# Kernel tuning notes

Hardware: AMD Instinct MI355X
Metric: run time of the kernel (lower is better)

The kernel has to match this reference:

```python
import jax, jax.numpy as jnp
import numpy as np

N = 100000
E = 1600000
IN_DIM = 128
HID = 128
C = 10
N_INJ = 20000
T_HET = 0.5          # self.hetero_level (set by set_adaptation_from_data)
HP_MAX = 1.0         # highpass_scale_max
INJ_LAM = 0.8        # self.inject_lambda


def setup_inputs() -> dict:
    key = jax.random.key(0)
    ks = jax.random.split(key, 16)
    glorot = lambda k, i, o: jax.random.normal(k, (i, o), jnp.float32) * (2.0 / (i + o)) ** 0.5
    return {
        "x": jax.random.normal(ks[0], (N, IN_DIM), jnp.float32),
        "edge_index": jax.random.randint(ks[1], (2, E), 0, N, jnp.int64),
        "inject_indices": jax.random.randint(ks[2], (N_INJ,), 0, N, jnp.int64),
        "initial_preds": jax.random.uniform(ks[3], (N, C), jnp.float32),
        "W1": glorot(ks[4], IN_DIM, HID), "b1": jnp.zeros((HID,), jnp.float32),
        "W2": glorot(ks[5], HID, HID),   "b2": jnp.zeros((HID,), jnp.float32),
        "Wl1": glorot(ks[6], IN_DIM, HID),
        "Wl2": glorot(ks[7], HID, HID),
        "Wm1": glorot(ks[8], HID, HID), "bm1": jnp.zeros((HID,), jnp.float32),
        "Wm2": glorot(ks[9], HID, C),   "bm2": jnp.zeros((C,), jnp.float32),
    }


def _gcn_norm(edge_index):
    # add self loops, symmetric D^{-1/2} (A+I) D^{-1/2} normalization (PyG GCNConv default)
    loops = jnp.arange(N, dtype=edge_index.dtype)
    src = jnp.concatenate([edge_index[0], loops])
    dst = jnp.concatenate([edge_index[1], loops])
    deg = jax.ops.segment_sum(jnp.ones_like(dst, jnp.float32), dst, num_segments=N)
    dinv = jnp.where(deg > 0, jax.lax.rsqrt(jnp.maximum(deg, 1.0)), 0.0)
    norm = dinv[src] * dinv[dst]  # [E+N]
    return src, dst, norm


def _gcn_conv(x, W, b, src, dst, norm):
    h = x @ W                                   # [N, H]
    msg = h[src] * norm[:, None]                # gather + scale, [E+N, H]
    return jax.ops.segment_sum(msg, dst, num_segments=N) + b


def reference(x, edge_index, inject_indices, initial_preds,
              W1, b1, W2, b2, Wl1, Wl2, Wm1, bm1, Wm2, bm2):
    src, dst, norm = _gcn_norm(edge_index)
    mix = T_HET * HP_MAX

    low1 = _gcn_conv(x, W1, b1, src, dst, norm)
    high1 = x @ Wl1 - low1
    h = jax.nn.relu(low1 + mix * high1)        # dropout: eval mode (identity)

    low2 = _gcn_conv(h, W2, b2, src, dst, norm)
    high2 = h @ Wl2 - low2
    h2 = low2 + mix * high2

    logits = jax.nn.relu(h2 @ Wm1 + bm1) @ Wm2 + bm2   # [N, C]
    # indexed injection: logits[idx] = logits[idx] + lam * preds[idx]
    logits = logits.at[inject_indices].set(
        logits[inject_indices] + INJ_LAM * initial_preds[inject_indices])
    return jax.nn.log_softmax(logits, axis=1)
```

## Files before the change

### kernel.cpp

```cpp
#include <hip/hip_runtime.h>
#include <hip/hip_bf16.h>
#include <math.h>

typedef __attribute__((ext_vector_type(8))) short short8;
typedef __attribute__((ext_vector_type(4))) float f32x4;
typedef __attribute__((ext_vector_type(2))) float f32x2;

#define INJ_LAM 0.8f
#define BSH 9
#define BWD 512

__device__ inline float bf2f(unsigned short s){
  union{unsigned u; float f;} v; v.u=((unsigned)s)<<16; return v.f;
}
__device__ inline unsigned short f2bf(float f){
  __hip_bfloat16 h=__float2bfloat16(f);
  return *reinterpret_cast<unsigned short*>(&h);
}
__device__ inline unsigned pack2(float lo, float hi){
  return ((unsigned)f2bf(hi)<<16)|(unsigned)f2bf(lo);
}

__global__ void k_bhist(const int* __restrict__ dst, unsigned* __restrict__ bhist8,
                        const int* __restrict__ inj, unsigned char* __restrict__ flag,
                        int E, int NI){
  __shared__ unsigned lh[256];
  int t=threadIdx.x;
  lh[t]=0u;
  int i=blockIdx.x*256+t;
  if(i<NI) flag[inj[i]]=1;
  __syncthreads();
  int base=blockIdx.x*2048;
  #pragma unroll
  for(int k=0;k<8;k++){
    int e=base+k*256+t;
    if(e<E) atomicAdd(&lh[dst[e]>>BSH],1u);
  }
  __syncthreads();
  if(lh[t]) atomicAdd(&bhist8[t*8],lh[t]);
}

__global__ void k_bscan(const unsigned* __restrict__ bhist8, unsigned* __restrict__ bbase,
                        unsigned* __restrict__ bcur8, int NBK){
  __shared__ unsigned ss[256];
  int t=threadIdx.x;
  unsigned v=(t<NBK)?bhist8[t*8]:0u;
  ss[t]=v; __syncthreads();
  for(int off=1;off<256;off<<=1){
    unsigned u=(t>=off)?ss[t-off]:0u; __syncthreads();
    ss[t]+=u; __syncthreads();
  }
  unsigned excl=ss[t]-v;
  if(t<NBK){ bbase[t]=excl; bcur8[t*8]=excl; }
  if(t==255) bbase[NBK]=ss[255];
}

__global__ void k_bscatter(const int* __restrict__ src, const int* __restrict__ dst,
                           unsigned* __restrict__ bcur8,
                           int* __restrict__ psrc, int* __restrict__ pdst, int E){
  __shared__ unsigned lh[256];
  __shared__ unsigned gb[256];
  int t=threadIdx.x;
  lh[t]=0u; __syncthreads();
  int base=blockIdx.x*2048;
  unsigned lr[8]; int bk[8], sv[8], dv_[8];
  #pragma unroll
  for(int k=0;k<8;k++){
    int e=base+k*256+t;
    if(e<E){
      int d=dst[e]; int b=d>>BSH;
      bk[k]=b; dv_[k]=d; sv[k]=src[e];
      lr[k]=atomicAdd(&lh[b],1u);
    } else bk[k]=-1;
  }
  __syncthreads();
  if(lh[t]) gb[t]=atomicAdd(&bcur8[t*8],lh[t]);
  __syncthreads();
  #pragma unroll
  for(int k=0;k<8;k++){
    if(bk[k]>=0){
      unsigned p=gb[bk[k]]+lr[k];
      psrc[p]=sv[k]; pdst[p]=dv_[k];
    }
  }
}

__launch_bounds__(256)
__global__ void k_bucket(const int* __restrict__ psrc, const int* __restrict__ pdst,
                         const unsigned* __restrict__ bbase, unsigned* __restrict__ rank,
                         unsigned* __restrict__ meta,
                         float* __restrict__ dinv, int* __restrict__ csr, int N){
  __shared__ unsigned lc[BWD];
  __shared__ unsigned lo[BWD];
  __shared__ unsigned ss[256];
  int b=blockIdx.x, t=threadIdx.x;
  unsigned e0=bbase[b], e1=bbase[b+1];
  int lo_node=b<<BSH;
  lc[t]=0u; lc[t+256]=0u; __syncthreads();
  for(unsigned p=e0+t;p<e1;p+=256){
    int dl=pdst[p]-lo_node;
    rank[p]=atomicAdd(&lc[dl],1u);
  }
  __syncthreads();
  unsigned c0=lc[2*t], c1=lc[2*t+1], ps=c0+c1;
  ss[t]=ps; __syncthreads();
  for(int off=1;off<256;off<<=1){
    unsigned u=(t>=off)?ss[t-off]:0u; __syncthreads();
    ss[t]+=u; __syncthreads();
  }
  unsigned excl=ss[t]-ps;
  lo[2*t]=excl; lo[2*t+1]=excl+c0;
  __syncthreads();
  #pragma unroll
  for(int k=0;k<2;k++){
    int nl=t+k*256; int node=lo_node+nl;
    if(node<N){
      unsigned c=lc[nl];
      meta[node]=(e0+lo[nl])|(c<<21);
      dinv[node]=rsqrtf((float)(c+1u));
    }
  }
  for(unsigned p=e0+t;p<e1;p+=256){
    int dl=pdst[p]-lo_node;
    csr[e0+lo[dl]+rank[p]]=psrc[p];
  }
}

__global__ void k_prepw(const float* __restrict__ W1,const float* __restrict__ Wl1,
                        const float* __restrict__ W2,const float* __restrict__ Wl2,
                        const float* __restrict__ Wm1,const float* __restrict__ Wm2,
                        const float* __restrict__ b1,const float* __restrict__ b2,
                        unsigned short* __restrict__ Wt1, unsigned short* __restrict__ Wt2,
                        unsigned short* __restrict__ Wm1t, unsigned short* __restrict__ Wm2tp,
                        float* __restrict__ bh1, float* __restrict__ bh2){
  int i=blockIdx.x*blockDim.x+threadIdx.x;
  if(i<256*128){
    int c=i>>7, k=i&127;
    float v1=(c<128)?W1[k*128+c]:Wl1[k*128+(c-128)];
    float v2=(c<128)?W2[k*128+c]:Wl2[k*128+(c-128)];
    Wt1[i]=f2bf(v1); Wt2[i]=f2bf(v2);
    if(c<128) Wm1t[i]=f2bf(Wm1[k*128+c]);
    if(c<16)  Wm2tp[i]=f2bf((c<10)?Wm2[k*10+c]:0.f);
    if(i<128){ bh1[i]=0.5f*b1[i]; bh2[i]=0.5f*b2[i]; }
  }
}

template<bool FP32IN>
__device__ inline void load_afrag(const void* __restrict__ Xv, size_t arow, int l4, short8* a){
  if(FP32IN){
    const float* X=(const float*)Xv + arow*128 + l4*8;
    #pragma unroll
    for(int ks=0;ks<4;ks++){
      float4 f0=*reinterpret_cast<const float4*>(X+ks*32);
      float4 f1=*reinterpret_cast<const float4*>(X+ks*32+4);
      short8 t;
      t[0]=(short)f2bf(f0.x); t[1]=(short)f2bf(f0.y); t[2]=(short)f2bf(f0.z); t[3]=(short)f2bf(f0.w);
      t[4]=(short)f2bf(f1.x); t[5]=(short)f2bf(f1.y); t[6]=(short)f2bf(f1.z); t[7]=(short)f2bf(f1.w);
      a[ks]=t;
    }
  }else{
    const unsigned short* X=(const unsigned short*)Xv + arow*128 + l4*8;
    #pragma unroll
    for(int ks=0;ks<4;ks++)
      a[ks]=*reinterpret_cast<const short8*>(X+ks*32);
  }
}

template<bool FP32IN>
__launch_bounds__(256, 4)
__global__ void k_gemm(const void* __restrict__ Xv, const unsigned short* __restrict__ Wt,
                       const float* __restrict__ dinv,
                       unsigned short* __restrict__ G, unsigned short* __restrict__ XL, int N){
  int wave=threadIdx.x>>6, lane=threadIdx.x&63;
  int l15=lane&15, l4=lane>>4;
  int blk0=blockIdx.x*128;
  if(blk0>=N) return;
  short8 wf[4][4];
  #pragma unroll
  for(int i=0;i<4;i++){
    int col=(wave*4+i)*16+l15;
    #pragma unroll
    for(int ks=0;ks<4;ks++)
      wf[i][ks]=*reinterpret_cast<const short8*>(Wt+(size_t)col*128+ks*32+l4*8);
  }
  int r0=blk0+l15; if(r0>N-1) r0=N-1;
  short8 aC[4], aN[4];
  load_afrag<FP32IN>(Xv,(size_t)r0,l4,aC);
  #pragma unroll 1
  for(int nt=0;nt<8;nt++){
    int node0=blk0+nt*16;
    if(node0>=N) break;
    if(nt<7){
      int rn=node0+16+l15; if(rn>N-1) rn=N-1;
      load_afrag<FP32IN>(Xv,(size_t)rn,l4,aN);
    }
    f32x4 acc[4];
    #pragma unroll
    for(int i=0;i<4;i++) acc[i]=(f32x4){0.f,0.f,0.f,0.f};
    #pragma unroll
    for(int i=0;i<4;i++){
      #pragma unroll
      for(int ks=0;ks<4;ks++)
        acc[i]=__builtin_amdgcn_mfma_f32_16x16x32_bf16(wf[i][ks],aC[ks],acc[i],0,0,0);
    }
    int node=node0+l15;
    if(node<N){
      if(wave<2){
        float dv=dinv[node];
        #pragma unroll
        for(int i=0;i<4;i++){
          f32x4 v=acc[i];
          uint2 p; p.x=pack2(v[0]*dv,v[1]*dv); p.y=pack2(v[2]*dv,v[3]*dv);
          *reinterpret_cast<uint2*>(G+(size_t)node*128+(wave*4+i)*16+l4*4)=p;
        }
      }else{
        #pragma unroll
        for(int i=0;i<4;i++){
          f32x4 v=acc[i];
          uint2 p; p.x=pack2(v[0]*0.5f,v[1]*0.5f); p.y=pack2(v[2]*0.5f,v[3]*0.5f);
          *reinterpret_cast<uint2*>(XL+(size_t)node*128+((wave-2)*4+i)*16+l4*4)=p;
        }
      }
    }
    #pragma unroll
    for(int ks=0;ks<4;ks++) aC[ks]=aN[ks];
  }
}

#define ADDQ(v) do{ \
  unsigned ux=(unsigned)(v).x, uy=(unsigned)(v).y, uz=(unsigned)(v).z, uw=(unsigned)(v).w; \
  accv[0]+=(f32x2){__uint_as_float(ux<<16),__uint_as_float(ux&0xffff0000u)}; \
  accv[1]+=(f32x2){__uint_as_float(uy<<16),__uint_as_float(uy&0xffff0000u)}; \
  accv[2]+=(f32x2){__uint_as_float(uz<<16),__uint_as_float(uz&0xffff0000u)}; \
  accv[3]+=(f32x2){__uint_as_float(uw<<16),__uint_as_float(uw&0xffff0000u)}; \
}while(0)

template<bool RELU>
__launch_bounds__(256)
__global__ void k_conv(const unsigned short* __restrict__ G, const unsigned short* __restrict__ XL,
                       const float* __restrict__ bh, const float* __restrict__ dinv,
                       const int* __restrict__ csr, const unsigned* __restrict__ meta,
                       unsigned short* __restrict__ H, int N){
  int node=blockIdx.x*4+(threadIdx.x>>6);
  if(node>=N) return;
  int lane=threadIdx.x&63;
  int g=lane>>4, li=lane&15;
  const int4* Gv=(const int4*)G;
  const int4 Z={0,0,0,0};
  f32x2 accv[4];
  #pragma unroll
  for(int i=0;i<4;i++) accv[i]=(f32x2){0.f,0.f};
  if(g==0){
    int4 v=Gv[(size_t)node*16+li];
    ADDQ(v);
  }
  unsigned mt=meta[node];
  unsigned start=mt&0x1FFFFFu, deg=mt>>21;
  unsigned j=(unsigned)g;
  int4 v0=Z,v1=Z,v2=Z,v3=Z;
  if(j<deg)    v0=Gv[(size_t)csr[start+j]*16+li];
  if(j+4<deg)  v1=Gv[(size_t)csr[start+j+4]*16+li];
  if(j+8<deg)  v2=Gv[(size_t)csr[start+j+8]*16+li];
  if(j+12<deg) v3=Gv[(size_t)csr[start+j+12]*16+li];
  j+=16;
  while(j<deg){
    int4 n0=Z,n1=Z,n2=Z,n3=Z;
    n0=Gv[(size_t)csr[start+j]*16+li];
    if(j+4<deg)  n1=Gv[(size_t)csr[start+j+4]*16+li];
    if(j+8<deg)  n2=Gv[(size_t)csr[start+j+8]*16+li];
    if(j+12<deg) n3=Gv[(size_t)csr[start+j+12]*16+li];
    ADDQ(v0); ADDQ(v1); ADDQ(v2); ADDQ(v3);
    v0=n0; v1=n1; v2=n2; v3=n3; j+=16;
  }
  ADDQ(v0); ADDQ(v1); ADDQ(v2); ADDQ(v3);
  float acc[8];
  #pragma unroll
  for(int i=0;i<4;i++){ acc[2*i]=accv[i][0]; acc[2*i+1]=accv[i][1]; }
  #pragma unroll
  for(int i=0;i<8;i++){
    acc[i]+=__shfl_xor(acc[i],16,64);
    acc[i]+=__shfl_xor(acc[i],32,64);
  }
  if(g==0){
    float dv2=0.5f*dinv[node];
    float4 b0=*reinterpret_cast<const float4*>(bh+li*8);
    float4 b1=*reinterpret_cast<const float4*>(bh+li*8+4);
    int4 xv=((const int4*)XL)[(size_t)node*16+li];
    float xl[8];
    { unsigned _x=(unsigned)xv.x,_y=(unsigned)xv.y,_z=(unsigned)xv.z,_w=(unsigned)xv.w;
      xl[0]=bf2f((unsigned short)(_x&0xffffu)); xl[1]=bf2f((unsigned short)(_x>>16));
      xl[2]=bf2f((unsigned short)(_y&0xffffu)); xl[3]=bf2f((unsigned short)(_y>>16));
      xl[4]=bf2f((unsigned short)(_z&0xffffu)); xl[5]=bf2f((unsigned short)(_z>>16));
      xl[6]=bf2f((unsigned short)(_w&0xffffu)); xl[7]=bf2f((unsigned short)(_w>>16)); }
    float bb[8]={b0.x,b0.y,b0.z,b0.w,b1.x,b1.y,b1.z,b1.w};
    float r[8];
    #pragma unroll
    for(int i=0;i<8;i++){
      r[i]=dv2*acc[i]+bb[i]+xl[i];
      if(RELU) r[i]=fmaxf(r[i],0.f);
    }
    int4 o;
    o.x=(int)pack2(r[0],r[1]); o.y=(int)pack2(r[2],r[3]);
    o.z=(int)pack2(r[4],r[5]); o.w=(int)pack2(r[6],r[7]);
    ((int4*)H)[(size_t)node*16+li]=o;
  }
}

__launch_bounds__(256)
__global__ void k_mlp(const unsigned short* __restrict__ H2,
                      const unsigned short* __restrict__ Wm1t,
                      const unsigned short* __restrict__ Wm2tp,
                      const float* __restrict__ bm1, const float* __restrict__ bm2,
                      const unsigned char* __restrict__ flag, const float* __restrict__ preds,
                      float* __restrict__ out, int N){
  __shared__ __align__(16) unsigned short zt[4][16][136];
  int wave=threadIdx.x>>6, lane=threadIdx.x&63;
  int l15=lane&15, l4=lane>>4;
  int node0=blockIdx.x*64+wave*16;
  int arow=node0+l15; if(arow>N-1) arow=N-1; if(arow<0) arow=0;
  short8 a[4];
  #pragma unroll
  for(int ks=0;ks<4;ks++)
    a[ks]=*reinterpret_cast<const short8*>(H2+(size_t)arow*128+ks*32+l4*8);
  f32x4 acc[8];
  #pragma unroll
  for(int ct=0;ct<8;ct++) acc[ct]=(f32x4){0.f,0.f,0.f,0.f};
  #pragma unroll
  for(int ct=0;ct<8;ct++){
    #pragma unroll
    for(int ks=0;ks<4;ks++){
      short8 bfr=*reinterpret_cast<const short8*>(Wm1t+(size_t)(ct*16+l15)*128+ks*32+l4*8);
      acc[ct]=__builtin_amdgcn_mfma_f32_16x16x32_bf16(bfr,a[ks],acc[ct],0,0,0);
    }
  }
  #pragma unroll
  for(int ct=0;ct<8;ct++){
    float4 bm=*reinterpret_cast<const float4*>(bm1+ct*16+l4*4);
    uint2 p;
    p.x=pack2(fmaxf(acc[ct][0]+bm.x,0.f),fmaxf(acc[ct][1]+bm.y,0.f));
    p.y=pack2(fmaxf(acc[ct][2]+bm.z,0.f),fmaxf(acc[ct][3]+bm.w,0.f));
    *reinterpret_cast<uint2*>(&zt[wave][l15][ct*16+l4*4])=p;
  }
  __syncthreads();
  short8 a2[4];
  #pragma unroll
  for(int ks=0;ks<4;ks++)
    a2[ks]=*reinterpret_cast<const short8*>(&zt[wave][l15][ks*32+l4*8]);
  f32x4 acc2=(f32x4){0.f,0.f,0.f,0.f};
  #pragma unroll
  for(int ks=0;ks<4;ks++){
    short8 bfr=*reinterpret_cast<const short8*>(Wm2tp+(size_t)l15*128+ks*32+l4*8);
    acc2=__builtin_amdgcn_mfma_f32_16x16x32_bf16(bfr,a2[ks],acc2,0,0,0);
  }
  int node=node0+l15;
  bool have=node<N;
  int c0=l4*4;
  float v[4];
  #pragma unroll
  for(int k=0;k<4;k++){
    int c=c0+k;
    v[k]=(c<10)?(acc2[k]+bm2[c]):-3.0e38f;
  }
  if(have && c0<10 && flag[node]){
    #pragma unroll
    for(int k=0;k<4;k++){
      int c=c0+k;
      if(c<10) v[k]+=INJ_LAM*preds[(size_t)node*10+c];
    }
  }
  float m=fmaxf(fmaxf(v[0],v[1]),fmaxf(v[2],v[3]));
  m=fmaxf(m,__shfl_xor(m,16,64));
  m=fmaxf(m,__shfl_xor(m,32,64));
  float s=0.f;
  #pragma unroll
  for(int k=0;k<4;k++){ int c=c0+k; if(c<10) s+=expf(v[k]-m); }
  s+=__shfl_xor(s,16,64);
  s+=__shfl_xor(s,32,64);
  float lse=m+logf(s);
  if(have && c0<10){
    float2 o01; o01.x=v[0]-lse; o01.y=v[1]-lse;
    *reinterpret_cast<float2*>(out+(size_t)node*10+c0)=o01;
    if(c0+2<10){
      float2 o23; o23.x=v[2]-lse; o23.y=v[3]-lse;
      *reinterpret_cast<float2*>(out+(size_t)node*10+c0+2)=o23;
    }
  }
}

extern "C" void kernel_launch(void* const* d_in, const int* in_sizes, int n_in,
                              void* d_out, int out_size, void* d_ws, size_t ws_size,
                              hipStream_t stream){
  const float* x    =(const float*)d_in[0];
  const int*   ei   =(const int*)  d_in[1];
  const int*   inj  =(const int*)  d_in[2];
  const float* preds=(const float*)d_in[3];
  const float* W1 =(const float*)d_in[4];  const float* b1 =(const float*)d_in[5];
  const float* W2 =(const float*)d_in[6];  const float* b2 =(const float*)d_in[7];
  const float* Wl1=(const float*)d_in[8];  const float* Wl2=(const float*)d_in[9];
  const float* Wm1=(const float*)d_in[10]; const float* bm1=(const float*)d_in[11];
  const float* Wm2=(const float*)d_in[12]; const float* bm2=(const float*)d_in[13];
  float* out=(float*)d_out;

  const int N  = in_sizes[0]/128;
  const int E  = in_sizes[1]/2;
  const int NI = in_sizes[2];
  const int* srcp = ei;
  const int* dstp = ei+E;
  const int NBK = (N+BWD-1)>>BSH;

  char* w=(char*)d_ws;
  auto carve=[&](size_t sz)->char*{ char* p=w; w+=(sz+255)&~(size_t)255; return p; };
  unsigned short* S0 =(unsigned short*)carve((size_t)N*128*2);
  unsigned short* S1 =(unsigned short*)carve((size_t)N*128*2);
  unsigned short* S2 =(unsigned short*)carve((size_t)N*128*2);
  unsigned short* Wt1=(unsigned short*)carve(256*128*2);
  unsigned short* Wt2=(unsigned short*)carve(256*128*2);
  unsigned short* Wm1t=(unsigned short*)carve(128*128*2);
  unsigned short* Wm2tp=(unsigned short*)carve(16*128*2);
  float*    dinv  =(float*)   carve((size_t)N*4);
  unsigned* meta  =(unsigned*)carve((size_t)N*4);
  int*      csr   =(int*)     carve((size_t)E*4);
  unsigned char* flags=(unsigned char*)carve(((size_t)N+3)&~(size_t)3);
  unsigned* bhist8=(unsigned*)carve(256*8*4);
  unsigned* bcur8 =(unsigned*)carve(256*8*4);
  unsigned* bbase =(unsigned*)carve(257*4);
  float* bh1=(float*)carve(128*4);
  float* bh2=(float*)carve(128*4);
  (void)ws_size; (void)n_in; (void)out_size;

  int* psrc=(int*)S1;
  int* pdst=psrc+E;
  unsigned* rank=(unsigned*)S2;

  const int T=256;
  const int EB=(E+2047)/2048;
  hipMemsetAsync(bhist8, 0, 256*8*4, stream);
  hipMemsetAsync(flags, 0, (size_t)N, stream);
  hipLaunchKernelGGL(k_bhist, dim3(EB), dim3(T), 0, stream, dstp, bhist8, inj, flags, E, NI);
  hipLaunchKernelGGL(k_bscan, dim3(1), dim3(T), 0, stream, bhist8, bbase, bcur8, NBK);
  hipLaunchKernelGGL(k_bscatter, dim3(EB), dim3(T), 0, stream, srcp, dstp, bcur8, psrc, pdst, E);
  hipLaunchKernelGGL(k_bucket, dim3(NBK), dim3(T), 0, stream, psrc, pdst, bbase, rank,
                     meta, dinv, csr, N);
  hipLaunchKernelGGL(k_prepw, dim3(128), dim3(T), 0, stream, W1,Wl1,W2,Wl2,Wm1,Wm2,b1,b2,
                     Wt1,Wt2,Wm1t,Wm2tp,bh1,bh2);

  dim3 gemmGrid((N+127)/128);
  hipLaunchKernelGGL(k_gemm<true>,  gemmGrid, dim3(T), 0, stream, (const void*)x,  Wt1, dinv, S1, S2, N);
  hipLaunchKernelGGL(k_conv<true>,  dim3((N+3)/4), dim3(T), 0, stream, S1, S2, bh1, dinv, csr, meta, S0, N);
  hipLaunchKernelGGL(k_gemm<false>, gemmGrid, dim3(T), 0, stream, (const void*)S0, Wt2, dinv, S1, S2, N);
  hipLaunchKernelGGL(k_conv<false>, dim3((N+3)/4), dim3(T), 0, stream, S1, S2, bh2, dinv, csr, meta, S0, N);
  hipLaunchKernelGGL(k_mlp, dim3((N+63)/64), dim3(T), 0, stream, S0, Wm1t, Wm2tp, bm1, bm2, flags, preds, out, N);
}
```

Before: 346.7 us.

## Fuse GCN aggregation with the following GEMM and MLP, and merge preprocessing kernels

Layer-1 aggregation now feeds a block-local shared-memory tile straight into the layer-2 weight GEMM (k_convg). Layer-2 aggregation likewise feeds the two-layer MLP and log-softmax (k_convm). This removes the separate k_gemm<false> and k_mlp launches and the round trips of N×128 bf16 activations through global memory. The memsets, the bucket scan and the injection-flag setup are folded into other kernels: each bscatter/bucket block redoes the 256-entry scan, and weight prep also zeroes the buffers. Buffers are reassigned so G2 overwrites the XL1 buffer in place. The risks are lower occupancy from 512-thread blocks doing both gather and MFMA work, and redundant per-block scans.

```diff
diff --git a/kernel.cpp b/kernel.cpp
--- a/kernel.cpp
+++ b/kernel.cpp
@@ -21,118 +21,15 @@
   return ((unsigned)f2bf(hi)<<16)|(unsigned)f2bf(lo);
 }
 
-__global__ void k_bhist(const int* __restrict__ dst, unsigned* __restrict__ bhist8,
-                        const int* __restrict__ inj, unsigned char* __restrict__ flag,
-                        int E, int NI){
-  __shared__ unsigned lh[256];
-  int t=threadIdx.x;
-  lh[t]=0u;
-  int i=blockIdx.x*256+t;
-  if(i<NI) flag[inj[i]]=1;
-  __syncthreads();
-  int base=blockIdx.x*2048;
-  #pragma unroll
-  for(int k=0;k<8;k++){
-    int e=base+k*256+t;
-    if(e<E) atomicAdd(&lh[dst[e]>>BSH],1u);
-  }
-  __syncthreads();
-  if(lh[t]) atomicAdd(&bhist8[t*8],lh[t]);
-}
-
-__global__ void k_bscan(const unsigned* __restrict__ bhist8, unsigned* __restrict__ bbase,
-                        unsigned* __restrict__ bcur8, int NBK){
-  __shared__ unsigned ss[256];
-  int t=threadIdx.x;
-  unsigned v=(t<NBK)?bhist8[t*8]:0u;
-  ss[t]=v; __syncthreads();
-  for(int off=1;off<256;off<<=1){
-    unsigned u=(t>=off)?ss[t-off]:0u; __syncthreads();
-    ss[t]+=u; __syncthreads();
-  }
-  unsigned excl=ss[t]-v;
-  if(t<NBK){ bbase[t]=excl; bcur8[t*8]=excl; }
-  if(t==255) bbase[NBK]=ss[255];
-}
-
-__global__ void k_bscatter(const int* __restrict__ src, const int* __restrict__ dst,
-                           unsigned* __restrict__ bcur8,
-                           int* __restrict__ psrc, int* __restrict__ pdst, int E){
-  __shared__ unsigned lh[256];
-  __shared__ unsigned gb[256];
-  int t=threadIdx.x;
-  lh[t]=0u; __syncthreads();
-  int base=blockIdx.x*2048;
-  unsigned lr[8]; int bk[8], sv[8], dv_[8];
-  #pragma unroll
-  for(int k=0;k<8;k++){
-    int e=base+k*256+t;
-    if(e<E){
-      int d=dst[e]; int b=d>>BSH;
-      bk[k]=b; dv_[k]=d; sv[k]=src[e];
-      lr[k]=atomicAdd(&lh[b],1u);
-    } else bk[k]=-1;
-  }
-  __syncthreads();
-  if(lh[t]) gb[t]=atomicAdd(&bcur8[t*8],lh[t]);
-  __syncthreads();
-  #pragma unroll
-  for(int k=0;k<8;k++){
-    if(bk[k]>=0){
-      unsigned p=gb[bk[k]]+lr[k];
-      psrc[p]=sv[k]; pdst[p]=dv_[k];
-    }
-  }
-}
-
-__launch_bounds__(256)
-__global__ void k_bucket(const int* __restrict__ psrc, const int* __restrict__ pdst,
-                         const unsigned* __restrict__ bbase, unsigned* __restrict__ rank,
-                         unsigned* __restrict__ meta,
-                         float* __restrict__ dinv, int* __restrict__ csr, int N){
-  __shared__ unsigned lc[BWD];
-  __shared__ unsigned lo[BWD];
-  __shared__ unsigned ss[256];
-  int b=blockIdx.x, t=threadIdx.x;
-  unsigned e0=bbase[b], e1=bbase[b+1];
-  int lo_node=b<<BSH;
-  lc[t]=0u; lc[t+256]=0u; __syncthreads();
-  for(unsigned p=e0+t;p<e1;p+=256){
-    int dl=pdst[p]-lo_node;
-    rank[p]=atomicAdd(&lc[dl],1u);
-  }
-  __syncthreads();
-  unsigned c0=lc[2*t], c1=lc[2*t+1], ps=c0+c1;
-  ss[t]=ps; __syncthreads();
-  for(int off=1;off<256;off<<=1){
-    unsigned u=(t>=off)?ss[t-off]:0u; __syncthreads();
-    ss[t]+=u; __syncthreads();
-  }
-  unsigned excl=ss[t]-ps;
-  lo[2*t]=excl; lo[2*t+1]=excl+c0;
-  __syncthreads();
-  #pragma unroll
-  for(int k=0;k<2;k++){
-    int nl=t+k*256; int node=lo_node+nl;
-    if(node<N){
-      unsigned c=lc[nl];
-      meta[node]=(e0+lo[nl])|(c<<21);
-      dinv[node]=rsqrtf((float)(c+1u));
-    }
-  }
-  for(unsigned p=e0+t;p<e1;p+=256){
-    int dl=pdst[p]-lo_node;
-    csr[e0+lo[dl]+rank[p]]=psrc[p];
-  }
-}
-
-__global__ void k_prepw(const float* __restrict__ W1,const float* __restrict__ Wl1,
-                        const float* __restrict__ W2,const float* __restrict__ Wl2,
-                        const float* __restrict__ Wm1,const float* __restrict__ Wm2,
-                        const float* __restrict__ b1,const float* __restrict__ b2,
-                        unsigned short* __restrict__ Wt1, unsigned short* __restrict__ Wt2,
-                        unsigned short* __restrict__ Wm1t, unsigned short* __restrict__ Wm2tp,
-                        float* __restrict__ bh1, float* __restrict__ bh2){
+__global__ void k_prep(const float* __restrict__ W1,const float* __restrict__ Wl1,
+                       const float* __restrict__ W2,const float* __restrict__ Wl2,
+                       const float* __restrict__ Wm1,const float* __restrict__ Wm2,
+                       const float* __restrict__ b1,const float* __restrict__ b2,
+                       unsigned short* __restrict__ Wt1, unsigned short* __restrict__ Wt2,
+                       unsigned short* __restrict__ Wm1t, unsigned short* __restrict__ Wm2tp,
+                       float* __restrict__ bh1, float* __restrict__ bh2,
+                       unsigned* __restrict__ flags32, int nf4,
+                       unsigned* __restrict__ bhist8, unsigned* __restrict__ zcur8){
   int i=blockIdx.x*blockDim.x+threadIdx.x;
   if(i<256*128){
     int c=i>>7, k=i&127;
@@ -142,6 +39,113 @@
     if(c<128) Wm1t[i]=f2bf(Wm1[k*128+c]);
     if(c<16)  Wm2tp[i]=f2bf((c<10)?Wm2[k*10+c]:0.f);
     if(i<128){ bh1[i]=0.5f*b1[i]; bh2[i]=0.5f*b2[i]; }
+  }
+  if(i<nf4) flags32[i]=0u;
+  if(i<2048){ bhist8[i]=0u; zcur8[i]=0u; }
+}
+
+__global__ void k_bhist(const int* __restrict__ dst, unsigned* __restrict__ bhist8, int E){
+  __shared__ unsigned lh[256];
+  int t=threadIdx.x;
+  lh[t]=0u; __syncthreads();
+  int base=blockIdx.x*2048;
+  #pragma unroll
+  for(int k=0;k<8;k++){
+    int e=base+k*256+t;
+    if(e<E) atomicAdd(&lh[dst[e]>>BSH],1u);
+  }
+  __syncthreads();
+  if(lh[t]) atomicAdd(&bhist8[t*8],lh[t]);
+}
+
+__launch_bounds__(256)
+__global__ void k_bscatter(const int* __restrict__ src, const int* __restrict__ dst,
+                           const unsigned* __restrict__ bhist8, unsigned* __restrict__ zcur8,
+                           int* __restrict__ psrc, int* __restrict__ pdst, int E, int NBK){
+  __shared__ unsigned lh[256];
+  __shared__ unsigned gb[256];
+  __shared__ unsigned ss[256];
+  int t=threadIdx.x;
+  lh[t]=0u;
+  unsigned v=(t<NBK)?bhist8[t*8]:0u;
+  ss[t]=v; __syncthreads();
+  for(int off=1;off<256;off<<=1){
+    unsigned u=(t>=off)?ss[t-off]:0u; __syncthreads();
+    ss[t]+=u; __syncthreads();
+  }
+  unsigned bb=ss[t]-v;
+  int base=blockIdx.x*2048;
+  unsigned lr[8]; int bk[8], sv[8], dv_[8];
+  #pragma unroll
+  for(int k=0;k<8;k++){
+    int e=base+k*256+t;
+    if(e<E){
+      int d=dst[e]; int b=d>>BSH;
+      bk[k]=b; dv_[k]=d; sv[k]=src[e];
+      lr[k]=atomicAdd(&lh[b],1u);
+    } else bk[k]=-1;
+  }
+  __syncthreads();
+  if(lh[t]) gb[t]=bb+atomicAdd(&zcur8[t*8],lh[t]);
+  __syncthreads();
+  #pragma unroll
+  for(int k=0;k<8;k++){
+    if(bk[k]>=0){
+      unsigned p=gb[bk[k]]+lr[k];
+      psrc[p]=sv[k]; pdst[p]=dv_[k];
+    }
+  }
+}
+
+__launch_bounds__(256)
+__global__ void k_bucket(const int* __restrict__ psrc, const int* __restrict__ pdst,
+                         const unsigned* __restrict__ bhist8, unsigned* __restrict__ rank,
+                         unsigned* __restrict__ meta, float* __restrict__ dinv,
+                         int* __restrict__ csr,
+                         const int* __restrict__ inj, unsigned char* __restrict__ flag,
+                         int N, int NI, int NBK){
+  __shared__ unsigned lc[BWD];
+  __shared__ unsigned lo[BWD];
+  __shared__ unsigned ss[256];
+  int b=blockIdx.x, t=threadIdx.x;
+  for(int i=b*256+t;i<NI;i+=gridDim.x*256) flag[inj[i]]=1;
+  unsigned v=(t<NBK)?bhist8[t*8]:0u;
+  ss[t]=v; lc[t]=0u; lc[t+256]=0u;
+  __syncthreads();
+  for(int off=1;off<256;off<<=1){
+    unsigned u=(t>=off)?ss[t-off]:0u; __syncthreads();
+    ss[t]+=u; __syncthreads();
+  }
+  unsigned e1=ss[b];
+  unsigned e0=e1-bhist8[b*8];
+  __syncthreads();
+  int lo_node=b<<BSH;
+  for(unsigned p=e0+t;p<e1;p+=256){
+    int dl=pdst[p]-lo_node;
+    rank[p]=atomicAdd(&lc[dl],1u);
+  }
+  __syncthreads();
+  unsigned c0=lc[2*t], c1=lc[2*t+1], ps=c0+c1;
+  ss[t]=ps; __syncthreads();
+  for(int off=1;off<256;off<<=1){
+    unsigned u=(t>=off)?ss[t-off]:0u; __syncthreads();
+    ss[t]+=u; __syncthreads();
+  }
+  unsigned excl=ss[t]-ps;
+  lo[2*t]=excl; lo[2*t+1]=excl+c0;
+  __syncthreads();
+  #pragma unroll
+  for(int k=0;k<2;k++){
+    int nl=t+k*256; int node=lo_node+nl;
+    if(node<N){
+      unsigned c=lc[nl];
+      meta[node]=(e0+lo[nl])|(c<<21);
+      dinv[node]=rsqrtf((float)(c+1u));
+    }
+  }
+  for(unsigned p=e0+t;p<e1;p+=256){
+    int dl=pdst[p]-lo_node;
+    csr[e0+lo[dl]+rank[p]]=psrc[p];
   }
 }
 
@@ -236,14 +240,12 @@
 }while(0)
 
 template<bool RELU>
-__launch_bounds__(256)
-__global__ void k_conv(const unsigned short* __restrict__ G, const unsigned short* __restrict__ XL,
-                       const float* __restrict__ bh, const float* __restrict__ dinv,
-                       const int* __restrict__ csr, const unsigned* __restrict__ meta,
-                       unsigned short* __restrict__ H, int N){
-  int node=blockIdx.x*4+(threadIdx.x>>6);
+__device__ __forceinline__ void conv_node(int node, int N,
+    const unsigned short* __restrict__ G, const unsigned short* __restrict__ XL,
+    const float* __restrict__ bh, const float* __restrict__ dinv,
+    const int* __restrict__ csr, const unsigned* __restrict__ meta,
+    unsigned short* __restrict__ ldsrow, int lane){
   if(node>=N) return;
-  int lane=threadIdx.x&63;
   int g=lane>>4, li=lane&15;
   const int4* Gv=(const int4*)G;
   const int4 Z={0,0,0,0};
@@ -302,87 +304,149 @@
     int4 o;
     o.x=(int)pack2(r[0],r[1]); o.y=(int)pack2(r[2],r[3]);
     o.z=(int)pack2(r[4],r[5]); o.w=(int)pack2(r[6],r[7]);
-    ((int4*)H)[(size_t)node*16+li]=o;
-  }
-}
-
-__launch_bounds__(256)
-__global__ void k_mlp(const unsigned short* __restrict__ H2,
-                      const unsigned short* __restrict__ Wm1t,
-                      const unsigned short* __restrict__ Wm2tp,
-                      const float* __restrict__ bm1, const float* __restrict__ bm2,
-                      const unsigned char* __restrict__ flag, const float* __restrict__ preds,
-                      float* __restrict__ out, int N){
-  __shared__ __align__(16) unsigned short zt[4][16][136];
+    *reinterpret_cast<int4*>(ldsrow+li*8)=o;
+  }
+}
+
+__launch_bounds__(512, 4)
+__global__ void k_convg(const unsigned short* __restrict__ G1, const unsigned short* __restrict__ XL1,
+                        const float* __restrict__ bh1, const float* __restrict__ dinv,
+                        const int* __restrict__ csr, const unsigned* __restrict__ meta,
+                        const unsigned short* __restrict__ Wt2,
+                        unsigned short* __restrict__ G2, unsigned short* __restrict__ XL2, int N){
+  __shared__ __align__(16) unsigned short ht[32][136];
   int wave=threadIdx.x>>6, lane=threadIdx.x&63;
   int l15=lane&15, l4=lane>>4;
-  int node0=blockIdx.x*64+wave*16;
-  int arow=node0+l15; if(arow>N-1) arow=N-1; if(arow<0) arow=0;
-  short8 a[4];
-  #pragma unroll
-  for(int ks=0;ks<4;ks++)
-    a[ks]=*reinterpret_cast<const short8*>(H2+(size_t)arow*128+ks*32+l4*8);
-  f32x4 acc[8];
-  #pragma unroll
-  for(int ct=0;ct<8;ct++) acc[ct]=(f32x4){0.f,0.f,0.f,0.f};
-  #pragma unroll
-  for(int ct=0;ct<8;ct++){
+  int blk0=blockIdx.x*32;
+  #pragma unroll 1
+  for(int it=0;it<4;it++){
+    int nl=it*8+wave;
+    conv_node<true>(blk0+nl, N, G1, XL1, bh1, dinv, csr, meta, &ht[nl][0], lane);
+  }
+  short8 wf[2][4];
+  #pragma unroll
+  for(int i=0;i<2;i++){
+    int col=(wave+i*8)*16+l15;
+    #pragma unroll
+    for(int ks=0;ks<4;ks++)
+      wf[i][ks]=*reinterpret_cast<const short8*>(Wt2+(size_t)col*128+ks*32+l4*8);
+  }
+  __syncthreads();
+  #pragma unroll
+  for(int q=0;q<2;q++){
+    short8 a[4];
+    #pragma unroll
+    for(int ks=0;ks<4;ks++)
+      a[ks]=*reinterpret_cast<const short8*>(&ht[q*16+l15][ks*32+l4*8]);
+    int node=blk0+q*16+l15;
+    float dv=(node<N)?dinv[node]:0.f;
+    #pragma unroll
+    for(int i=0;i<2;i++){
+      f32x4 acc=(f32x4){0.f,0.f,0.f,0.f};
+      #pragma unroll
+      for(int ks=0;ks<4;ks++)
+        acc=__builtin_amdgcn_mfma_f32_16x16x32_bf16(wf[i][ks],a[ks],acc,0,0,0);
+      if(node<N){
+        int ct=wave+i*8;
+        if(ct<8){
+          uint2 p; p.x=pack2(acc[0]*dv,acc[1]*dv); p.y=pack2(acc[2]*dv,acc[3]*dv);
+          *reinterpret_cast<uint2*>(G2+(size_t)node*128+ct*16+l4*4)=p;
+        }else{
+          uint2 p; p.x=pack2(acc[0]*0.5f,acc[1]*0.5f); p.y=pack2(acc[2]*0.5f,acc[3]*0.5f);
+          *reinterpret_cast<uint2*>(XL2+(size_t)node*128+(ct-8)*16+l4*4)=p;
+        }
+      }
+    }
+  }
+}
+
+__launch_bounds__(512, 4)
+__global__ void k_convm(const unsigned short* __restrict__ G2, const unsigned short* __restrict__ XL2,
+                        const float* __restrict__ bh2, const float* __restrict__ dinv,
+                        const int* __restrict__ csr, const unsigned* __restrict__ meta,
+                        const unsigned short* __restrict__ Wm1t, const unsigned short* __restrict__ Wm2tp,
+                        const float* __restrict__ bm1, const float* __restrict__ bm2,
+                        const unsigned char* __restrict__ flag, const float* __restrict__ preds,
+                        float* __restrict__ out, int N){
+  __shared__ __align__(16) unsigned short ht[32][136];
+  __shared__ __align__(16) unsigned short zt[32][136];
+  int wave=threadIdx.x>>6, lane=threadIdx.x&63;
+  int l15=lane&15, l4=lane>>4;
+  int blk0=blockIdx.x*32;
+  #pragma unroll 1
+  for(int it=0;it<4;it++){
+    int nl=it*8+wave;
+    conv_node<false>(blk0+nl, N, G2, XL2, bh2, dinv, csr, meta, &ht[nl][0], lane);
+  }
+  short8 wf1[4];
+  {
+    int col=wave*16+l15;
+    #pragma unroll
+    for(int ks=0;ks<4;ks++)
+      wf1[ks]=*reinterpret_cast<const short8*>(Wm1t+(size_t)col*128+ks*32+l4*8);
+  }
+  __syncthreads();
+  #pragma unroll
+  for(int q=0;q<2;q++){
+    short8 a[4];
+    #pragma unroll
+    for(int ks=0;ks<4;ks++)
+      a[ks]=*reinterpret_cast<const short8*>(&ht[q*16+l15][ks*32+l4*8]);
+    f32x4 acc=(f32x4){0.f,0.f,0.f,0.f};
+    #pragma unroll
+    for(int ks=0;ks<4;ks++)
+      acc=__builtin_amdgcn_mfma_f32_16x16x32_bf16(wf1[ks],a[ks],acc,0,0,0);
+    float4 bm=*reinterpret_cast<const float4*>(bm1+wave*16+l4*4);
+    uint2 p;
+    p.x=pack2(fmaxf(acc[0]+bm.x,0.f),fmaxf(acc[1]+bm.y,0.f));
+    p.y=pack2(fmaxf(acc[2]+bm.z,0.f),fmaxf(acc[3]+bm.w,0.f));
+    *reinterpret_cast<uint2*>(&zt[q*16+l15][wave*16+l4*4])=p;
+  }
+  __syncthreads();
+  if(wave<2){
+    int q=wave;
+    short8 a2[4], w2[4];
     #pragma unroll
     for(int ks=0;ks<4;ks++){
-      short8 bfr=*reinterpret_cast<const short8*>(Wm1t+(size_t)(ct*16+l15)*128+ks*32+l4*8);
-      acc[ct]=__builtin_amdgcn_mfma_f32_16x16x32_bf16(bfr,a[ks],acc[ct],0,0,0);
-    }
-  }
-  #pragma unroll
-  for(int ct=0;ct<8;ct++){
-    float4 bm=*reinterpret_cast<const float4*>(bm1+ct*16+l4*4);
-    uint2 p;
-    p.x=pack2(fmaxf(acc[ct][0]+bm.x,0.f),fmaxf(acc[ct][1]+bm.y,0.f));
-    p.y=pack2(fmaxf(acc[ct][2]+bm.z,0.f),fmaxf(acc[ct][3]+bm.w,0.f));
-    *reinterpret_cast<uint2*>(&zt[wave][l15][ct*16+l4*4])=p;
-  }
-  __syncthreads();
-  short8 a2[4];
-  #pragma unroll
-  for(int ks=0;ks<4;ks++)
-    a2[ks]=*reinterpret_cast<const short8*>(&zt[wave][l15][ks*32+l4*8]);
-  f32x4 acc2=(f32x4){0.f,0.f,0.f,0.f};
-  #pragma unroll
-  for(int ks=0;ks<4;ks++){
-    short8 bfr=*reinterpret_cast<const short8*>(Wm2tp+(size_t)l15*128+ks*32+l4*8);
-    acc2=__builtin_amdgcn_mfma_f32_16x16x32_bf16(bfr,a2[ks],acc2,0,0,0);
-  }
-  int node=node0+l15;
-  bool have=node<N;
-  int c0=l4*4;
-  float v[4];
-  #pragma unroll
-  for(int k=0;k<4;k++){
-    int c=c0+k;
-    v[k]=(c<10)?(acc2[k]+bm2[c]):-3.0e38f;
-  }
-  if(have && c0<10 && flag[node]){
+      a2[ks]=*reinterpret_cast<const short8*>(&zt[q*16+l15][ks*32+l4*8]);
+      w2[ks]=*reinterpret_cast<const short8*>(Wm2tp+(size_t)l15*128+ks*32+l4*8);
+    }
+    f32x4 acc2=(f32x4){0.f,0.f,0.f,0.f};
+    #pragma unroll
+    for(int ks=0;ks<4;ks++)
+      acc2=__builtin_amdgcn_mfma_f32_16x16x32_bf16(w2[ks],a2[ks],acc2,0,0,0);
+    int node=blk0+q*16+l15;
+    bool have=node<N;
+    int c0=l4*4;
+    float v[4];
     #pragma unroll
     for(int k=0;k<4;k++){
       int c=c0+k;
-      if(c<10) v[k]+=INJ_LAM*preds[(size_t)node*10+c];
-    }
-  }
-  float m=fmaxf(fmaxf(v[0],v[1]),fmaxf(v[2],v[3]));
-  m=fmaxf(m,__shfl_xor(m,16,64));
-  m=fmaxf(m,__shfl_xor(m,32,64));
-  float s=0.f;
-  #pragma unroll
-  for(int k=0;k<4;k++){ int c=c0+k; if(c<10) s+=expf(v[k]-m); }
-  s+=__shfl_xor(s,16,64);
-  s+=__shfl_xor(s,32,64);
-  float lse=m+logf(s);
-  if(have && c0<10){
-    float2 o01; o01.x=v[0]-lse; o01.y=v[1]-lse;
-    *reinterpret_cast<float2*>(out+(size_t)node*10+c0)=o01;
-    if(c0+2<10){
-      float2 o23; o23.x=v[2]-lse; o23.y=v[3]-lse;
-      *reinterpret_cast<float2*>(out+(size_t)node*10+c0+2)=o23;
+      v[k]=(c<10)?(acc2[k]+bm2[c]):-3.0e38f;
+    }
+    if(have && c0<10 && flag[node]){
+      #pragma unroll
+      for(int k=0;k<4;k++){
+        int c=c0+k;
+        if(c<10) v[k]+=INJ_LAM*preds[(size_t)node*10+c];
+      }
+    }
+    float m=fmaxf(fmaxf(v[0],v[1]),fmaxf(v[2],v[3]));
+    m=fmaxf(m,__shfl_xor(m,16,64));
+    m=fmaxf(m,__shfl_xor(m,32,64));
+    float s=0.f;
+    #pragma unroll
+    for(int k=0;k<4;k++){ int c=c0+k; if(c<10) s+=expf(v[k]-m); }
+    s+=__shfl_xor(s,16,64);
+    s+=__shfl_xor(s,32,64);
+    float lse=m+logf(s);
+    if(have && c0<10){
+      float2 o01; o01.x=v[0]-lse; o01.y=v[1]-lse;
+      *reinterpret_cast<float2*>(out+(size_t)node*10+c0)=o01;
+      if(c0+2<10){
+        float2 o23; o23.x=v[2]-lse; o23.y=v[3]-lse;
+        *reinterpret_cast<float2*>(out+(size_t)node*10+c0+2)=o23;
+      }
     }
   }
 }
@@ -410,9 +474,9 @@
 
   char* w=(char*)d_ws;
   auto carve=[&](size_t sz)->char*{ char* p=w; w+=(sz+255)&~(size_t)255; return p; };
-  unsigned short* S0 =(unsigned short*)carve((size_t)N*128*2);
   unsigned short* S1 =(unsigned short*)carve((size_t)N*128*2);
   unsigned short* S2 =(unsigned short*)carve((size_t)N*128*2);
+  unsigned short* S3 =(unsigned short*)carve((size_t)N*128*2);
   unsigned short* Wt1=(unsigned short*)carve(256*128*2);
   unsigned short* Wt2=(unsigned short*)carve(256*128*2);
   unsigned short* Wm1t=(unsigned short*)carve(128*128*2);
@@ -422,32 +486,33 @@
   int*      csr   =(int*)     carve((size_t)E*4);
   unsigned char* flags=(unsigned char*)carve(((size_t)N+3)&~(size_t)3);
   unsigned* bhist8=(unsigned*)carve(256*8*4);
-  unsigned* bcur8 =(unsigned*)carve(256*8*4);
-  unsigned* bbase =(unsigned*)carve(257*4);
+  unsigned* zcur8 =(unsigned*)carve(256*8*4);
   float* bh1=(float*)carve(128*4);
   float* bh2=(float*)carve(128*4);
   (void)ws_size; (void)n_in; (void)out_size;
 
-  int* psrc=(int*)S1;
+  int* psrc=(int*)S3;
   int* pdst=psrc+E;
-  unsigned* rank=(unsigned*)S2;
+  unsigned* rank=(unsigned*)S1;
 
   const int T=256;
   const int EB=(E+2047)/2048;
-  hipMemsetAsync(bhist8, 0, 256*8*4, stream);
-  hipMemsetAsync(flags, 0, (size_t)N, stream);
-  hipLaunchKernelGGL(k_bhist, dim3(EB), dim3(T), 0, stream, dstp, bhist8, inj, flags, E, NI);
-  hipLaunchKernelGGL(k_bscan, dim3(1), dim3(T), 0, stream, bhist8, bbase, bcur8, NBK);
-  hipLaunchKernelGGL(k_bscatter, dim3(EB), dim3(T), 0, stream, srcp, dstp, bcur8, psrc, pdst, E);
-  hipLaunchKernelGGL(k_bucket, dim3(NBK), dim3(T), 0, stream, psrc, pdst, bbase, rank,
-                     meta, dinv, csr, N);
-  hipLaunchKernelGGL(k_prepw, dim3(128), dim3(T), 0, stream, W1,Wl1,W2,Wl2,Wm1,Wm2,b1,b2,
-                     Wt1,Wt2,Wm1t,Wm2tp,bh1,bh2);
-
-  dim3 gemmGrid((N+127)/128);
-  hipLaunchKernelGGL(k_gemm<true>,  gemmGrid, dim3(T), 0, stream, (const void*)x,  Wt1, dinv, S1, S2, N);
-  hipLaunchKernelGGL(k_conv<true>,  dim3((N+3)/4), dim3(T), 0, stream, S1, S2, bh1, dinv, csr, meta, S0, N);
-  hipLaunchKernelGGL(k_gemm<false>, gemmGrid, dim3(T), 0, stream, (const void*)S0, Wt2, dinv, S1, S2, N);
-  hipLaunchKernelGGL(k_conv<false>, dim3((N+3)/4), dim3(T), 0, stream, S1, S2, bh2, dinv, csr, meta, S0, N);
-  hipLaunchKernelGGL(k_mlp, dim3((N+63)/64), dim3(T), 0, stream, S0, Wm1t, Wm2tp, bm1, bm2, flags, preds, out, N);
-}
+  const int nf4=(N+3)/4;
+  int gp=(32768>nf4?32768:nf4); gp=(gp+T-1)/T;
+  hipLaunchKernelGGL(k_prep, dim3(gp), dim3(T), 0, stream,
+                     W1,Wl1,W2,Wl2,Wm1,Wm2,b1,b2,
+                     Wt1,Wt2,Wm1t,Wm2tp,bh1,bh2,
+                     (unsigned*)flags, nf4, bhist8, zcur8);
+  hipLaunchKernelGGL(k_bhist, dim3(EB), dim3(T), 0, stream, dstp, bhist8, E);
+  hipLaunchKernelGGL(k_bscatter, dim3(EB), dim3(T), 0, stream, srcp, dstp, bhist8, zcur8,
+                     psrc, pdst, E, NBK);
+  hipLaunchKernelGGL(k_bucket, dim3(NBK), dim3(T), 0, stream, psrc, pdst, bhist8, rank,
+                     meta, dinv, csr, inj, flags, N, NI, NBK);
+  hipLaunchKernelGGL(k_gemm<true>, dim3((N+127)/128), dim3(T), 0, stream,
+                     (const void*)x, Wt1, dinv, S1, S2, N);
+  hipLaunchKernelGGL(k_convg, dim3((N+31)/32), dim3(512), 0, stream,
+                     S1, S2, bh1, dinv, csr, meta, Wt2, S2, S3, N);
+  hipLaunchKernelGGL(k_convm, dim3((N+31)/32), dim3(512), 0, stream,
+                     S2, S3, bh2, dinv, csr, meta, Wm1t, Wm2tp, bm1, bm2,
+                     flags, preds, out, N);
+}
```

Result: faster. 332.1 us (-4.2%).
